# Performance work log

Measured on AMD Instinct MI355X. Metric: run time of the kernel, lower is better.

## Reference

```python
import jax, jax.numpy as jnp
import numpy as np

N = 131072          # num MCMC chains (num_samples)
N_STEPS = 60        # sample_mcmc default n_steps
EPS_INIT = 10.0     # sample_mcmc default eps_init
H = 128             # hidden width of the energy MLP


def setup_inputs() -> dict:
    key = jax.random.key(0)
    ks = jax.random.split(key, 8)
    d = {}
    # init points uniform in [-1, 1] (mimics the fresh-sample branch / buffer contents)
    d["x0"] = jax.random.uniform(ks[0], (N, 2), jnp.float32, minval=-1.0, maxval=1.0)
    # MLP 2 -> 128 -> 128 -> 128 -> 128 -> 1 (Kaiming-ish scale)
    def init_w(k, shape):
        fan_in = shape[0]
        return jax.random.normal(k, shape, jnp.float32) / jnp.sqrt(jnp.float32(fan_in))
    d["w1"] = init_w(ks[1], (2, H));  d["b1"] = jnp.zeros((H,), jnp.float32)
    d["w2"] = init_w(ks[2], (H, H));  d["b2"] = jnp.zeros((H,), jnp.float32)
    d["w3"] = init_w(ks[3], (H, H));  d["b3"] = jnp.zeros((H,), jnp.float32)
    d["w4"] = init_w(ks[4], (H, H));  d["b4"] = jnp.zeros((H,), jnp.float32)
    d["w5"] = init_w(ks[5], (H, 1));  d["b5"] = jnp.zeros((1,), jnp.float32)
    # pre-drawn Langevin noise for each of the 60 steps (torch.randn_like per step)
    d["noise"] = jax.random.normal(ks[6], (N_STEPS, N, 2), jnp.float32)
    return d


def _energy(x, params):
    # nn.Sequential(Linear, SiLU, Linear, SiLU, Linear, SiLU, Linear, SiLU, Linear)
    w1, b1, w2, b2, w3, b3, w4, b4, w5, b5 = params
    h = jax.nn.silu(x @ w1 + b1)
    h = jax.nn.silu(h @ w2 + b2)
    h = jax.nn.silu(h @ w3 + b3)
    h = jax.nn.silu(h @ w4 + b4)
    return h @ w5 + b5  # [N, 1]


def reference(x0, w1, b1, w2, b2, w3, b3, w4, b4, w5, b5, noise):
    params = (w1, b1, w2, b2, w3, b3, w4, b4, w5, b5)
    # grad of sum of energies wrt x == per-sample dE/dx
    grad_fn = jax.grad(lambda x: _energy(x, params).sum())

    def step(x, inp):
        i, nz = inp
        eps = EPS_INIT * (1.0 - i / N_STEPS)  # eps_init - eps_init*step/n_steps
        # torch.autograd.grad (create_graph=False) -> detached grad
        g = jnp.clip(jax.lax.stop_gradient(grad_fn(x)), -0.03, 0.03)
        x = jnp.clip(x + jnp.sqrt(2.0 * eps) * nz * 0.005 + eps * g, -2.43, 3.05)
        return x, None

    steps = jnp.arange(N_STEPS, dtype=jnp.float32)
    x, _ = jax.lax.scan(step, x0, (steps, noise))
    return x
```

## Files before the change

kernel.cpp:

```cpp
#include <hip/hip_runtime.h>
#include <stdint.h>

#define NTOT    131072
#define NSTEP   60
#define SBLK    32
#define NBLK    (NTOT / SBLK)
#define PLANE_H 16384
#define IMG_H   32768
#define BPLANE_H 4096

#define OFF_ACT0 0
#define OFF_ACT1 16384
#define OFF_GP   32768
#define OFF_W1C  33792
#define OFF_B2   35840
#define OFF_B3   36352
#define OFF_B4   36864
#define OFF_W5   37376
#define LDS_TOTAL 37888

typedef float  f32x4  __attribute__((ext_vector_type(4)));
typedef float  f32x16 __attribute__((ext_vector_type(16)));
typedef short  bf16x8 __attribute__((ext_vector_type(8)));
union FragU { bf16x8 v; uint32_t u[4]; uint16_t h[8]; };

static __device__ __forceinline__ uint32_t rne_bits(float f) {
  uint32_t u = __float_as_uint(f);
  return u + 0x7fffu + ((u >> 16) & 1u);
}
static __device__ __forceinline__ float fsigm(float z) {
  return __builtin_amdgcn_rcpf(1.0f + __builtin_amdgcn_exp2f(z * -1.44269504089f));
}
static __device__ __forceinline__ uint32_t cvt_pk_bf16(float a, float b) {
  uint32_t r;
  asm("v_cvt_pk_bf16_f32 %0, %1, %2" : "=v"(r) : "v"(a), "v"(b));
  return r;
}

extern "C" __global__ void ebm_prep_kernel(const float* __restrict__ w2,
                                           const float* __restrict__ w3,
                                           const float* __restrict__ w4,
                                           uint16_t* __restrict__ ws) {
  int img = blockIdx.x;
  bool bwd = img >= 3;
  int li = bwd ? 5 - img : img;
  const float* w = (li == 0) ? w2 : (li == 1) ? w3 : w4;
  uint16_t* hiP = ws + (size_t)img * IMG_H;
  uint16_t* loP = hiP + PLANE_H;
  for (int e = threadIdx.x; e < 16384; e += blockDim.x) {
    int i = e >> 7, o = e & 127;
    int m = bwd ? i : o;
    int k = bwd ? o : i;
    int slot = ((m >> 5) * 8 + (k >> 4)) * 64 + (m & 31) + 32 * ((k >> 3) & 1);
    int off = slot * 8 + (k & 7);
    float v = w[e];
    uint32_t tb = rne_bits(v);
    float lo = v - __uint_as_float(tb & 0xffff0000u);
    hiP[off] = (uint16_t)(tb >> 16);
    loP[off] = (uint16_t)(rne_bits(lo) >> 16);
  }
}

extern "C" __global__ void __launch_bounds__(256, 2)
ebm_mcmc_kernel(const float* __restrict__ x0, const float* __restrict__ w1,
                const float* __restrict__ b1, const float* __restrict__ b2,
                const float* __restrict__ b3, const float* __restrict__ b4,
                const float* __restrict__ w5, const float* __restrict__ noise,
                const uint16_t* __restrict__ wsW, float* __restrict__ out)
{
  extern __shared__ char smem[];
  uint16_t* ACT0  = (uint16_t*)(smem + OFF_ACT0);
  uint16_t* ACT1  = (uint16_t*)(smem + OFF_ACT1);
  float*    GPf   = (float*)(smem + OFF_GP);
  float2*   GPf2  = (float2*)(smem + OFF_GP);
  f32x4*    W1C   = (f32x4*)(smem + OFF_W1C);
  float*    B2s   = (float*)(smem + OFF_B2);
  float*    B3s   = (float*)(smem + OFF_B3);
  float*    B4s   = (float*)(smem + OFF_B4);
  float*    W5s   = (float*)(smem + OFF_W5);

  const int t   = threadIdx.x;
  const int blk = blockIdx.x;

  if (t < 128) {
    f32x4 v; v.x = w1[t]; v.y = w1[128 + t]; v.z = b1[t]; v.w = 0.0f;
    W1C[t] = v;
    B2s[t] = b2[t]; B3s[t] = b3[t]; B4s[t] = b4[t]; W5s[t] = w5[t];
  }

  const int lane = t & 63;
  const int wave = t >> 6;
  const int c32 = lane & 31;
  const int h   = lane >> 5;
  const int wr  = wave;

  const int gs32 = blk * 32 + c32;
  const float2* x02 = (const float2*)x0;
  const float2* nz2 = (const float2*)noise;
  float2* out2 = (float2*)out;
  float2 x  = x02[gs32];
  float2 nz = nz2[gs32];

  __syncthreads();

  f32x16 acc;
  float D1[16], D2[16], D3[16];

  auto gemm = [&](int img, const uint16_t* AB) {
    const uint16_t* ab = wsW + (size_t)img * IMG_H + (size_t)(wr * 4096 + lane * 8);
    acc = (f32x16)0.0f;
#pragma unroll
    for (int ks = 0; ks < 8; ++ks) {
      FragU Ah, Al;
      Ah.v = *(const bf16x8*)(ab + ks * 512);
      Al.v = *(const bf16x8*)(ab + ks * 512 + PLANE_H);
      const uint16_t* bp = AB + (ks * 64 + lane) * 8;
      FragU Bh, Bl;
      Bh.v = *(const bf16x8*)bp;
      Bl.v = *(const bf16x8*)(bp + BPLANE_H);
      acc = __builtin_amdgcn_mfma_f32_32x32x16_bf16(Ah.v, Bh.v, acc, 0, 0, 0);
      acc = __builtin_amdgcn_mfma_f32_32x32x16_bf16(Ah.v, Bl.v, acc, 0, 0, 0);
      acc = __builtin_amdgcn_mfma_f32_32x32x16_bf16(Al.v, Bh.v, acc, 0, 0, 0);
    }
  };

  auto storeAct = [&](uint16_t* AB, int tt, f32x4 v) {
    uint32_t h01 = cvt_pk_bf16(v[0], v[1]);
    uint32_t h23 = cvt_pk_bf16(v[2], v[3]);
    float r0 = v[0] - __uint_as_float(h01 << 16);
    float r1 = v[1] - __uint_as_float(h01 & 0xffff0000u);
    float r2 = v[2] - __uint_as_float(h23 << 16);
    float r3 = v[3] - __uint_as_float(h23 & 0xffff0000u);
    int slot = (2 * wr + (tt >> 1)) * 64 + c32 + 32 * (tt & 1);
    uint16_t* p = AB + slot * 8 + 4 * h;
    *(uint2*)p = make_uint2(h01, h23);
    *(uint2*)(p + BPLANE_H) = make_uint2(cvt_pk_bf16(r0, r1), cvt_pk_bf16(r2, r3));
  };

  auto ep_fwd = [&](const float* Bs, float* D, uint16_t* AB) {
#pragma unroll
    for (int tt = 0; tt < 4; ++tt) {
      f32x4 bv = *(const f32x4*)(Bs + 32 * wr + 8 * tt + 4 * h);
      f32x4 hv;
#pragma unroll
      for (int rr = 0; rr < 4; ++rr) {
        float z = acc[4 * tt + rr] + bv[rr];
        float s = fsigm(z);
        float hh = z * s;
        D[4 * tt + rr] = s * (1.0f + z - hh);
        hv[rr] = hh;
      }
      storeAct(AB, tt, hv);
    }
  };

  auto ep_v4 = [&](uint16_t* AB) {
#pragma unroll
    for (int tt = 0; tt < 4; ++tt) {
      f32x4 bv = *(const f32x4*)(B4s + 32 * wr + 8 * tt + 4 * h);
      f32x4 wv = *(const f32x4*)(W5s + 32 * wr + 8 * tt + 4 * h);
      f32x4 vv;
#pragma unroll
      for (int rr = 0; rr < 4; ++rr) {
        float z = acc[4 * tt + rr] + bv[rr];
        float s = fsigm(z);
        vv[rr] = wv[rr] * (s * (1.0f + z - z * s));
      }
      storeAct(AB, tt, vv);
    }
  };

  auto ep_bwd = [&](float* D, uint16_t* AB) {
#pragma unroll
    for (int tt = 0; tt < 4; ++tt) {
      f32x4 vv;
#pragma unroll
      for (int rr = 0; rr < 4; ++rr)
        vv[rr] = acc[4 * tt + rr] * D[4 * tt + rr];
      storeAct(AB, tt, vv);
    }
  };

  auto ep_bwd1 = [&]() {
    float gx = 0.f, gy = 0.f;
#pragma unroll
    for (int tt = 0; tt < 4; ++tt) {
      const f32x4* wp = W1C + 32 * wr + 8 * tt + 4 * h;
#pragma unroll
      for (int rr = 0; rr < 4; ++rr) {
        f32x4 w = wp[rr];
        float v = acc[4 * tt + rr] * D1[4 * tt + rr];
        gx = fmaf(v, w.x, gx);
        gy = fmaf(v, w.y, gy);
      }
    }
    gx += __shfl_xor(gx, 32);
    gy += __shfl_xor(gy, 32);
    if (h == 0) {
      *(float2*)(GPf + (wr * 32 + c32) * 2) = make_float2(gx, gy);
    }
  };

  auto l1_phase = [&](uint16_t* AB) {
    float2 xv = x;
#pragma unroll
    for (int tt = 0; tt < 4; ++tt) {
      const f32x4* wp = W1C + 32 * wr + 8 * tt + 4 * h;
      f32x4 hv;
#pragma unroll
      for (int rr = 0; rr < 4; ++rr) {
        f32x4 w = wp[rr];
        float z = fmaf(xv.x, w.x, fmaf(xv.y, w.y, w.z));
        float s = fsigm(z);
        float hh = z * s;
        D1[4 * tt + rr] = s * (1.0f + z - hh);
        hv[rr] = hh;
      }
      storeAct(AB, tt, hv);
    }
  };

  auto g_update = [&](int step) {
    float2 g0 = GPf2[c32], g1 = GPf2[32 + c32];
    float2 g2 = GPf2[64 + c32], g3 = GPf2[96 + c32];
    float gxs = ((g0.x + g1.x) + g2.x) + g3.x;
    float gys = ((g0.y + g1.y) + g2.y) + g3.y;
    gxs = fminf(fmaxf(gxs, -0.03f), 0.03f);
    gys = fminf(fmaxf(gys, -0.03f), 0.03f);
    float epsv = 10.0f * (1.0f - (float)step / 60.0f);
    float sq = sqrtf(2.0f * epsv);
    x.x = fminf(fmaxf(x.x + sq * nz.x * 0.005f + epsv * gxs, -2.43f), 3.05f);
    x.y = fminf(fmaxf(x.y + sq * nz.y * 0.005f + epsv * gys, -2.43f), 3.05f);
    if (step == NSTEP - 1) {
      if (wave == 0 && h == 0) out2[gs32] = x;
    } else {
      nz = nz2[(size_t)(step + 1) * NTOT + gs32];
    }
  };

#pragma unroll 1
  for (int step = 0; step < NSTEP; ++step) {
    l1_phase(ACT0);                       __syncthreads();
    gemm(0, ACT0); ep_fwd(B2s, D2, ACT1); __syncthreads();
    gemm(1, ACT1); ep_fwd(B3s, D3, ACT0); __syncthreads();
    gemm(2, ACT0); ep_v4(ACT1);           __syncthreads();
    gemm(3, ACT1); ep_bwd(D3, ACT0);      __syncthreads();
    gemm(4, ACT0); ep_bwd(D2, ACT1);      __syncthreads();
    gemm(5, ACT1); ep_bwd1();             __syncthreads();
    g_update(step);
  }
}

extern "C" void kernel_launch(void* const* d_in, const int* in_sizes, int n_in,
                              void* d_out, int out_size, void* d_ws, size_t ws_size,
                              hipStream_t stream) {
  (void)in_sizes; (void)n_in; (void)out_size; (void)ws_size;
  hipFuncSetAttribute((const void*)ebm_mcmc_kernel,
                      hipFuncAttributeMaxDynamicSharedMemorySize, LDS_TOTAL);
  ebm_prep_kernel<<<6, 256, 0, stream>>>(
      (const float*)d_in[3], (const float*)d_in[5], (const float*)d_in[7],
      (uint16_t*)d_ws);
  ebm_mcmc_kernel<<<NBLK, 256, LDS_TOTAL, stream>>>(
      (const float*)d_in[0], (const float*)d_in[1], (const float*)d_in[2],
      (const float*)d_in[4], (const float*)d_in[6], (const float*)d_in[8],
      (const float*)d_in[9], (const float*)d_in[11], (const uint16_t*)d_ws,
      (float*)d_out);
}
```

Baseline: 6.296 ms.

## Spill SiLU derivatives to LDS and single-buffer activations to raise occupancy

Moves the per-layer SiLU derivative arrays D2/D3 out of registers into LDS and replaces the double-buffered activation tiles with a single buffer. This frees VGPRs so launch bounds can be raised from 2 to 3 blocks per CU. The price is twice as many block barriers per step, since every GEMM and epilogue is now separated by a sync, plus extra LDS traffic for the derivatives. The total LDS footprint also grows.

```diff
diff --git a/kernel.cpp b/kernel.cpp
--- a/kernel.cpp
+++ b/kernel.cpp
@@ -9,15 +9,16 @@
 #define IMG_H   32768
 #define BPLANE_H 4096
 
-#define OFF_ACT0 0
-#define OFF_ACT1 16384
-#define OFF_GP   32768
-#define OFF_W1C  33792
-#define OFF_B2   35840
-#define OFF_B3   36352
-#define OFF_B4   36864
-#define OFF_W5   37376
-#define LDS_TOTAL 37888
+#define OFF_ACT  0
+#define OFF_D2   16384
+#define OFF_D3   32768
+#define OFF_GP   49152
+#define OFF_W1C  50176
+#define OFF_B2   52224
+#define OFF_B3   52736
+#define OFF_B4   53248
+#define OFF_W5   53760
+#define LDS_TOTAL 54272
 
 typedef float  f32x4  __attribute__((ext_vector_type(4)));
 typedef float  f32x16 __attribute__((ext_vector_type(16)));
@@ -61,7 +62,7 @@
   }
 }
 
-extern "C" __global__ void __launch_bounds__(256, 2)
+extern "C" __global__ void __launch_bounds__(256, 3)
 ebm_mcmc_kernel(const float* __restrict__ x0, const float* __restrict__ w1,
                 const float* __restrict__ b1, const float* __restrict__ b2,
                 const float* __restrict__ b3, const float* __restrict__ b4,
@@ -69,8 +70,9 @@
                 const uint16_t* __restrict__ wsW, float* __restrict__ out)
 {
   extern __shared__ char smem[];
-  uint16_t* ACT0  = (uint16_t*)(smem + OFF_ACT0);
-  uint16_t* ACT1  = (uint16_t*)(smem + OFF_ACT1);
+  uint16_t* ACT   = (uint16_t*)(smem + OFF_ACT);
+  float*    D2L   = (float*)(smem + OFF_D2);
+  float*    D3L   = (float*)(smem + OFF_D3);
   float*    GPf   = (float*)(smem + OFF_GP);
   float2*   GPf2  = (float2*)(smem + OFF_GP);
   f32x4*    W1C   = (f32x4*)(smem + OFF_W1C);
@@ -104,9 +106,9 @@
   __syncthreads();
 
   f32x16 acc;
-  float D1[16], D2[16], D3[16];
-
-  auto gemm = [&](int img, const uint16_t* AB) {
+  float D1[16];
+
+  auto gemm = [&](int img) {
     const uint16_t* ab = wsW + (size_t)img * IMG_H + (size_t)(wr * 4096 + lane * 8);
     acc = (f32x16)0.0f;
 #pragma unroll
@@ -114,7 +116,7 @@
       FragU Ah, Al;
       Ah.v = *(const bf16x8*)(ab + ks * 512);
       Al.v = *(const bf16x8*)(ab + ks * 512 + PLANE_H);
-      const uint16_t* bp = AB + (ks * 64 + lane) * 8;
+      const uint16_t* bp = ACT + (ks * 64 + lane) * 8;
       FragU Bh, Bl;
       Bh.v = *(const bf16x8*)bp;
       Bl.v = *(const bf16x8*)(bp + BPLANE_H);
@@ -124,7 +126,7 @@
     }
   };
 
-  auto storeAct = [&](uint16_t* AB, int tt, f32x4 v) {
+  auto storeAct = [&](int tt, f32x4 v) {
     uint32_t h01 = cvt_pk_bf16(v[0], v[1]);
     uint32_t h23 = cvt_pk_bf16(v[2], v[3]);
     float r0 = v[0] - __uint_as_float(h01 << 16);
@@ -132,12 +134,12 @@
     float r2 = v[2] - __uint_as_float(h23 << 16);
     float r3 = v[3] - __uint_as_float(h23 & 0xffff0000u);
     int slot = (2 * wr + (tt >> 1)) * 64 + c32 + 32 * (tt & 1);
-    uint16_t* p = AB + slot * 8 + 4 * h;
+    uint16_t* p = ACT + slot * 8 + 4 * h;
     *(uint2*)p = make_uint2(h01, h23);
     *(uint2*)(p + BPLANE_H) = make_uint2(cvt_pk_bf16(r0, r1), cvt_pk_bf16(r2, r3));
   };
 
-  auto ep_fwd = [&](const float* Bs, float* D, uint16_t* AB) {
+  auto ep_fwd = [&](const float* Bs, float* Dl) {
 #pragma unroll
     for (int tt = 0; tt < 4; ++tt) {
       f32x4 bv = *(const f32x4*)(Bs + 32 * wr + 8 * tt + 4 * h);
@@ -147,14 +149,14 @@
         float z = acc[4 * tt + rr] + bv[rr];
         float s = fsigm(z);
         float hh = z * s;
-        D[4 * tt + rr] = s * (1.0f + z - hh);
+        Dl[(tt * 4 + rr) * 256 + t] = s * (1.0f + z - hh);
         hv[rr] = hh;
       }
-      storeAct(AB, tt, hv);
-    }
-  };
-
-  auto ep_v4 = [&](uint16_t* AB) {
+      storeAct(tt, hv);
+    }
+  };
+
+  auto ep_v4 = [&]() {
 #pragma unroll
     for (int tt = 0; tt < 4; ++tt) {
       f32x4 bv = *(const f32x4*)(B4s + 32 * wr + 8 * tt + 4 * h);
@@ -166,18 +168,18 @@
         float s = fsigm(z);
         vv[rr] = wv[rr] * (s * (1.0f + z - z * s));
       }
-      storeAct(AB, tt, vv);
-    }
-  };
-
-  auto ep_bwd = [&](float* D, uint16_t* AB) {
+      storeAct(tt, vv);
+    }
+  };
+
+  auto ep_bwd = [&](const float* Dl) {
 #pragma unroll
     for (int tt = 0; tt < 4; ++tt) {
       f32x4 vv;
 #pragma unroll
       for (int rr = 0; rr < 4; ++rr)
-        vv[rr] = acc[4 * tt + rr] * D[4 * tt + rr];
-      storeAct(AB, tt, vv);
+        vv[rr] = acc[4 * tt + rr] * Dl[(tt * 4 + rr) * 256 + t];
+      storeAct(tt, vv);
     }
   };
 
@@ -201,7 +203,7 @@
     }
   };
 
-  auto l1_phase = [&](uint16_t* AB) {
+  auto l1_phase = [&]() {
     float2 xv = x;
 #pragma unroll
     for (int tt = 0; tt < 4; ++tt) {
@@ -216,7 +218,7 @@
         D1[4 * tt + rr] = s * (1.0f + z - hh);
         hv[rr] = hh;
       }
-      storeAct(AB, tt, hv);
+      storeAct(tt, hv);
     }
   };
 
@@ -240,13 +242,19 @@
 
 #pragma unroll 1
   for (int step = 0; step < NSTEP; ++step) {
-    l1_phase(ACT0);                       __syncthreads();
-    gemm(0, ACT0); ep_fwd(B2s, D2, ACT1); __syncthreads();
-    gemm(1, ACT1); ep_fwd(B3s, D3, ACT0); __syncthreads();
-    gemm(2, ACT0); ep_v4(ACT1);           __syncthreads();
-    gemm(3, ACT1); ep_bwd(D3, ACT0);      __syncthreads();
-    gemm(4, ACT0); ep_bwd(D2, ACT1);      __syncthreads();
-    gemm(5, ACT1); ep_bwd1();             __syncthreads();
+    l1_phase();          __syncthreads();
+    gemm(0);             __syncthreads();
+    ep_fwd(B2s, D2L);    __syncthreads();
+    gemm(1);             __syncthreads();
+    ep_fwd(B3s, D3L);    __syncthreads();
+    gemm(2);             __syncthreads();
+    ep_v4();             __syncthreads();
+    gemm(3);             __syncthreads();
+    ep_bwd(D3L);         __syncthreads();
+    gemm(4);             __syncthreads();
+    ep_bwd(D2L);         __syncthreads();
+    gemm(5);             __syncthreads();
+    ep_bwd1();           __syncthreads();
     g_update(step);
   }
 }
```

New measurement: 8.377 ms. +33.1%, slower.
